# Kernel optimization log

Hardware: AMD Instinct MI355X
Metric: run time of the kernel (lower is better)

The kernel has to match this reference:

```python
import jax, jax.numpy as jnp
import numpy as np

EPS = 1e-5
NEG_SLOPE = 0.01


def _bn_eval(x, gamma, beta, mean, var):
    # x: [B, C, T], per-channel inference batchnorm
    inv = jax.lax.rsqrt(var + EPS)
    return gamma[:, None] * (x - mean[:, None]) * inv[:, None] + beta[:, None]


def _spp_max(x, L, num_levels):
    """Vectorized ragged spatial pyramid max-pool.
    x: [B, C, T] (valid data for sample b lives in [0, L[b]))
    L: [B] int effective lengths (= orig_len - shift)
    Level lvl has W=2**lvl windows: window j covers [j*floor(L/W), j*floor(L/W)+ceil(L/W)),
    matching F.max_pool1d(kernel=ceil(L/W), stride=floor(L/W)).
    Output layout per torch .view(e): channel-major -> [B, C*W] per level, levels concatenated.
    """
    B, C, T = x.shape
    t = jnp.arange(T)
    outs = []
    for lvl in range(num_levels):
        W = 2 ** lvl
        s = L // W                      # stride  = floor(L / 2^lvl)
        k = (L + W - 1) // W            # kernel  = ceil(L / 2^lvl)
        j = jnp.arange(W)
        start = j[None, :] * s[:, None]                        # [B, W]
        end = jnp.minimum(start + k[:, None], L[:, None])      # [B, W]
        m = (t[None, None, :] >= start[:, :, None]) & (t[None, None, :] < end[:, :, None])  # [B, W, T]
        vals = jnp.where(m[:, :, None, :], x[:, None, :, :], -jnp.inf)  # [B, W, C, T]
        pooled = vals.max(axis=-1)                             # [B, W, C]
        outs.append(pooled.transpose(0, 2, 1).reshape(B, C * W))
    return jnp.concatenate(outs, axis=1)


def setup_inputs() -> dict:
    key = jax.random.key(0)
    ks = jax.random.split(key, 8)
    B, C, T, K, n_levels, n_tasks = 32, 128, 8192, 21, 2, 2
    n_lin = 2 * C * (2 ** n_levels - 1)
    x = jax.random.normal(ks[0], (B, C, T), dtype=jnp.float32)
    orig_len = jax.random.randint(ks[1], (B,), 1024, T + 1)
    conv1_w = jax.random.normal(ks[2], (C, C, K), dtype=jnp.float32) * (1.0 / np.sqrt(C * K))
    bn1_gamma = jnp.ones((C,), jnp.float32)
    bn1_beta = jnp.zeros((C,), jnp.float32)
    bn1_mean = jax.random.normal(ks[3], (C,), dtype=jnp.float32) * 0.1
    bn1_var = jax.random.uniform(ks[4], (C,), dtype=jnp.float32, minval=0.5, maxval=1.5)
    fc_w = jax.random.normal(ks[5], (n_tasks, n_lin), dtype=jnp.float32) * (1.0 / np.sqrt(n_lin))
    fc_b = jnp.zeros((n_tasks,), jnp.float32)
    return {"x": x, "orig_len": orig_len, "conv1_w": conv1_w, "bn1_gamma": bn1_gamma,
            "bn1_beta": bn1_beta, "bn1_mean": bn1_mean, "bn1_var": bn1_var,
            "fc_w": fc_w, "fc_b": fc_b}


def reference(x, orig_len, conv1_w, bn1_gamma, bn1_beta, bn1_mean, bn1_var, fc_w, fc_b):
    K = conv1_w.shape[-1]
    n_levels = 2
    # original forward uses conv1/bn1 for BOTH branches (conv2/bn2 dead code)
    h = jax.lax.conv_general_dilated(x, conv1_w, window_strides=(1,), padding='VALID',
                                     dimension_numbers=('NCH', 'OIH', 'NCH'))  # [B, C, T-K+1]
    h = jax.nn.leaky_relu(_bn_eval(h, bn1_gamma, bn1_beta, bn1_mean, bn1_var), NEG_SLOPE)
    x1 = _spp_max(h, orig_len - (K - 1), n_levels)       # spp1: shift = K-1
    x2 = _spp_max(h, orig_len - 2 * (K - 1), n_levels)   # spp2: shift = 2*(K-1)
    feat = jnp.concatenate([x1, x2], axis=1)             # [B, 6C]
    return feat @ fc_w.T + fc_b
```

## Files before the change

kernel.cpp:

```cpp
#include <hip/hip_runtime.h>


typedef __attribute__((ext_vector_type(4))) float f32x4;
typedef __attribute__((ext_vector_type(4))) int i32x4;
typedef unsigned short u16;
typedef unsigned int u32;
typedef signed char i8;

#define T_SZ 8192
#define C_SZ 128
#define B_SZ 32
#define KW 21
#define FEAT 768
#define SX 25.4f
#define IMIN (-2147483647 - 1)

#define XT_OFF  0
#define WP_OFF  33554432u
#define BNA_OFF 33898496u
#define BNB_OFF 33899008u
#define FK_OFF  33899520u
#define PT_OFF  33997824u

__device__ __forceinline__ u32 fkey(float f) {
  u32 u = __float_as_uint(f);
  return (u & 0x80000000u) ? ~u : (u | 0x80000000u);
}
__device__ __forceinline__ float funkey(u32 k) {
  u32 u = (k & 0x80000000u) ? (k ^ 0x80000000u) : ~k;
  return __uint_as_float(u);
}

__device__ __forceinline__ i8 q8(float v) {
  v = fminf(fmaxf(v, -127.f), 127.f);
  return (i8)__float2int_rn(v);
}

__device__ __forceinline__ void gload_lds16(void* lds, const void* g) {
  __builtin_amdgcn_global_load_lds(
      (const __attribute__((address_space(1))) u32*)g,
      (__attribute__((address_space(3))) u32*)lds, 16, 0, 0);
}

__global__ void k_absmax(const float* __restrict__ W, float* __restrict__ parts) {
  const int i0 = ((int)blockIdx.x * 256 + (int)threadIdx.x) * 4;
  float m = 0.f;
#pragma unroll
  for (int j = 0; j < 4; ++j) m = fmaxf(m, fabsf(W[i0 + j]));
#pragma unroll
  for (int d = 1; d < 64; d <<= 1) m = fmaxf(m, __shfl_xor(m, d));
  if ((threadIdx.x & 63) == 0)
    parts[blockIdx.x * 4 + (threadIdx.x >> 6)] = m;
}

__device__ __forceinline__ float reduce_parts(const float* __restrict__ parts,
                                              float* lds4) {
  float m = 0.f;
  for (int i = (int)threadIdx.x; i < 1344; i += 256) m = fmaxf(m, parts[i]);
#pragma unroll
  for (int d = 1; d < 64; d <<= 1) m = fmaxf(m, __shfl_xor(m, d));
  if (((int)threadIdx.x & 63) == 0) lds4[(int)threadIdx.x >> 6] = m;
  __syncthreads();
  return fmaxf(fmaxf(lds4[0], lds4[1]), fmaxf(lds4[2], lds4[3]));
}

__global__ void k_fused(const float* __restrict__ X, const float* __restrict__ W,
                        const float* __restrict__ g, const float* __restrict__ be,
                        const float* __restrict__ mn, const float* __restrict__ vr,
                        const float* __restrict__ parts,
                        i8* __restrict__ Xt, i8* __restrict__ Wp,
                        float* __restrict__ bnA, float* __restrict__ bnB,
                        u32* __restrict__ feat) {
  __shared__ float smem[C_SZ * 65];
  const int tid = (int)threadIdx.x;
  const int bid = (int)blockIdx.x;

  if (bid < 4096) {
    const int b = bid >> 7;
    const int t0 = (bid & 127) * 64;
    const float* Xb = X + (size_t)b * C_SZ * T_SZ;
    {
      const int cw = tid >> 4;
      const int ch = tid & 15;
#pragma unroll
      for (int it = 0; it < 8; ++it) {
        const int ci = it * 16 + cw;
        const f32x4 v = *(const f32x4*)&Xb[(size_t)ci * T_SZ + t0 + ch * 4];
        smem[ci * 65 + ch * 4 + 0] = v.x;
        smem[ci * 65 + ch * 4 + 1] = v.y;
        smem[ci * 65 + ch * 4 + 2] = v.z;
        smem[ci * 65 + ch * 4 + 3] = v.w;
      }
    }
    __syncthreads();
    const int t = tid >> 2;
    const int q = tid & 3;
    u32 dw[8];
#pragma unroll
    for (int d = 0; d < 8; ++d) {
      u32 w = 0;
#pragma unroll
      for (int jb = 0; jb < 4; ++jb) {
        const int j = d * 4 + jb;
        const float v = smem[(q * 32 + j) * 65 + t] * SX;
        w |= ((u32)(unsigned char)q8(v)) << (jb * 8);
      }
      dw[d] = w;
    }
    u32* dst = (u32*)(Xt + ((size_t)(b * T_SZ + t0 + t)) * C_SZ + q * 32);
    *(i32x4*)(dst + 0) = (i32x4){(int)dw[0], (int)dw[1], (int)dw[2], (int)dw[3]};
    *(i32x4*)(dst + 4) = (i32x4){(int)dw[4], (int)dw[5], (int)dw[6], (int)dw[7]};
  } else if (bid == 4096) {
    const float wmax = reduce_parts(parts, smem);
    if (tid < C_SZ) {
      const float sw = 127.f / wmax;
      const float invS = 1.f / (SX * sw);
      float inv = rsqrtf(vr[tid] + 1e-5f);
      float a = g[tid] * inv;
      bnA[tid] = a * invS;
      bnB[tid] = be[tid] - a * mn[tid];
    }
    for (int i = tid; i < B_SZ * FEAT; i += 256) feat[i] = 0u;
  } else {
    const float wmax = reduce_parts(parts, smem);
    const float sw = 127.f / wmax;
    const int i = (bid - 4097) * 256 + tid;
    const int e = i & 15;
    const int lane = (i >> 4) & 63;
    const int f = (i >> 10) & 7;
    const int wr = (i >> 13) & 1;
    const int k = i >> 14;
    const int m = f & 3, ks = f >> 2;
    const int co = wr * 64 + m * 16 + (lane & 15);
    const int ci = ks * 64 + (lane >> 4) * 16 + e;
    Wp[i] = q8(W[(co * C_SZ + ci) * KW + k] * sw);
  }
}

__global__ __launch_bounds__(256, 2)
void k_conv(const i8* __restrict__ Xt, const i8* __restrict__ Wp,
            const float* __restrict__ bnA, const float* __restrict__ bnB,
            const int* __restrict__ olen, u32* __restrict__ feat) {
  __shared__ __align__(16) i8 Xs[280 * C_SZ];
  __shared__ int parti[2][4][C_SZ];

  const int tid = (int)threadIdx.x;
  const int wid = tid >> 6, lane = tid & 63;
  const int wr = wid >> 1, wc = wid & 1;
  const int l4 = lane & 15, lh = lane >> 4;
  const int b = (int)blockIdx.y;
  const int t0 = (int)blockIdx.x * 256;

  i32x4 av[2][4];
  {
    const i8* wb = Wp + ((size_t)wr << 13) + (lane << 4);
#pragma unroll
    for (int f = 0; f < 8; ++f)
      av[f >> 2][f & 3] = *(const i32x4*)&wb[f << 10];
  }

  {
    const i8* xb = Xt + (size_t)b * T_SZ * C_SZ;
    for (int i = wid; i < 35; i += 4) {
      int trow = t0 + i * 8 + (lane >> 3);
      trow = trow < T_SZ ? trow : (T_SZ - 1);
      const i8* src = xb + (size_t)trow * C_SZ + (((lane & 7) ^ (trow & 7)) << 4);
      gload_lds16(&Xs[i * 1024], src);
    }
  }
  __syncthreads();

  i32x4 acc[4][8];
#pragma unroll
  for (int m = 0; m < 4; ++m)
#pragma unroll
    for (int n = 0; n < 8; ++n) acc[m][n] = (i32x4){0, 0, 0, 0};

  const int rowc = wc * 128 + l4;
#pragma unroll 3
  for (int k = 0; k < KW; ++k) {
    const int kn = (k + 1 < KW) ? (k + 1) : k;
    const int rowb = rowc + k;
    const i8* wbn = Wp + (((size_t)(kn * 2 + wr)) << 13) + (lane << 4);
#pragma unroll
    for (int ks = 0; ks < 2; ++ks) {
      const int gran = ((ks << 2) + lh) ^ (rowb & 7);
      const i8* xp = &Xs[(rowb << 7) + (gran << 4)];
      i32x4 bv[8];
#pragma unroll
      for (int n = 0; n < 8; ++n)
        bv[n] = *(const i32x4*)&xp[n << 11];
      __builtin_amdgcn_s_setprio(1);
#pragma unroll
      for (int m = 0; m < 4; ++m)
#pragma unroll
        for (int n = 0; n < 8; ++n)
          acc[m][n] = __builtin_amdgcn_mfma_i32_16x16x64_i8(
              av[ks][m], bv[n], acc[m][n], 0, 0, 0);
      __builtin_amdgcn_s_setprio(0);
#pragma unroll
      for (int m = 0; m < 4; ++m)
        av[ks][m] = *(const i32x4*)&wbn[((ks << 2) + m) << 10];
    }
  }

  const int len = olen[b];
  const int L1 = len - (KW - 1);
  const int L2 = len - 2 * (KW - 1);
  int wlo[4], whi[4];
  wlo[0] = 0;       whi[0] = (L1 + 1) >> 1;
  wlo[1] = L1 >> 1; whi[1] = L1;
  wlo[2] = 0;       whi[2] = (L2 + 1) >> 1;
  wlo[3] = L2 >> 1; whi[3] = L2;

  int tg[8];
#pragma unroll
  for (int n = 0; n < 8; ++n) tg[n] = t0 + wc * 128 + n * 16 + l4;

#pragma unroll
  for (int w = 0; w < 4; ++w) {
    bool pr[8];
#pragma unroll
    for (int n = 0; n < 8; ++n) pr[n] = (tg[n] >= wlo[w]) & (tg[n] < whi[w]);
#pragma unroll
    for (int m = 0; m < 4; ++m)
#pragma unroll
      for (int r = 0; r < 4; ++r) {
        int mx = IMIN;
#pragma unroll
        for (int n = 0; n < 8; ++n)
          mx = max(mx, pr[n] ? acc[m][n][r] : IMIN);
#pragma unroll
        for (int d = 1; d < 16; d <<= 1) mx = max(mx, __shfl_xor(mx, d));
        if (l4 == 0) parti[wc][w][wr * 64 + m * 16 + lh * 4 + r] = mx;
      }
  }
  __syncthreads();
  if (tid < C_SZ) {
    const int c = tid;
    const int v1 = max(parti[0][0][c], parti[1][0][c]);
    const int v2 = max(parti[0][1][c], parti[1][1][c]);
    const int v4 = max(parti[0][2][c], parti[1][2][c]);
    const int v5 = max(parti[0][3][c], parti[1][3][c]);
    const int v0 = max(v1, v2);
    const int v3 = max(v4, v5);
    const float a = bnA[c], bb = bnB[c];
    u32* fb_ = feat + b * FEAT;
    float h;
    h = a * (float)v0 + bb; h = h > 0.f ? h : 0.01f * h;
    atomicMax(&fb_[c], fkey(h));
    h = a * (float)v1 + bb; h = h > 0.f ? h : 0.01f * h;
    atomicMax(&fb_[128 + 2 * c], fkey(h));
    h = a * (float)v2 + bb; h = h > 0.f ? h : 0.01f * h;
    atomicMax(&fb_[129 + 2 * c], fkey(h));
    h = a * (float)v3 + bb; h = h > 0.f ? h : 0.01f * h;
    atomicMax(&fb_[384 + c], fkey(h));
    h = a * (float)v4 + bb; h = h > 0.f ? h : 0.01f * h;
    atomicMax(&fb_[512 + 2 * c], fkey(h));
    h = a * (float)v5 + bb; h = h > 0.f ? h : 0.01f * h;
    atomicMax(&fb_[513 + 2 * c], fkey(h));
  }
}

__global__ void k_fc(const u32* __restrict__ feat, const float* __restrict__ fw,
                     const float* __restrict__ fb, float* __restrict__ out) {
  const int bj = (int)blockIdx.x;
  const int b = bj >> 1, j = bj & 1;
  const int lane = (int)threadIdx.x;
  float s = 0.f;
  for (int i = lane; i < FEAT; i += 64)
    s += funkey(feat[b * FEAT + i]) * fw[j * FEAT + i];
#pragma unroll
  for (int d = 1; d < 64; d <<= 1) s += __shfl_xor(s, d);
  if (lane == 0) out[b * 2 + j] = s + fb[j];
}

extern "C" void kernel_launch(void* const* d_in, const int* in_sizes, int n_in,
                              void* d_out, int out_size, void* d_ws, size_t ws_size,
                              hipStream_t stream) {
  (void)in_sizes; (void)n_in; (void)out_size; (void)ws_size;
  const float* x     = (const float*)d_in[0];
  const int*   olen  = (const int*)d_in[1];
  const float* w     = (const float*)d_in[2];
  const float* gamma = (const float*)d_in[3];
  const float* beta  = (const float*)d_in[4];
  const float* mean  = (const float*)d_in[5];
  const float* var   = (const float*)d_in[6];
  const float* fw    = (const float*)d_in[7];
  const float* fb    = (const float*)d_in[8];
  float* out = (float*)d_out;

  char* ws = (char*)d_ws;
  i8*  Xt    = (i8*)(ws + XT_OFF);
  i8*  Wp    = (i8*)(ws + WP_OFF);
  float* bnA  = (float*)(ws + BNA_OFF);
  float* bnB  = (float*)(ws + BNB_OFF);
  u32* feat  = (u32*)(ws + FK_OFF);
  float* parts = (float*)(ws + PT_OFF);

  k_absmax<<<336, 256, 0, stream>>>(w, parts);
  k_fused<<<4097 + 1344, 256, 0, stream>>>(x, w, gamma, beta, mean, var, parts,
                                           Xt, Wp, bnA, bnB, feat);
  k_conv<<<dim3(T_SZ / 256, B_SZ), 256, 0, stream>>>(Xt, Wp, bnA, bnB, olen, feat);
  k_fc<<<64, 64, 0, stream>>>(feat, fw, fb, out);
}
```

Baseline: 120.1 us.

## Repartition conv waves to cover all output channels over 64 time steps

Changes the wave tiling of the int8 MFMA conv from a 2x2 grid (64 channels x 128 time steps per wave) to four waves each computing all 128 output channels over 64 time steps. Each wave now holds the full weight slice in registers, so the number of LDS reads of the input tile per MFMA is halved. The next-k weight reloads are interleaved into the MFMA loop per row instead of issued after it. In exchange, each wave issues twice as many global weight loads and carries more weight registers, and the partial-max reduction grows from 2 to 4 partials.

```diff
diff --git a/kernel.cpp b/kernel.cpp
--- a/kernel.cpp
+++ b/kernel.cpp
@@ -142,26 +142,27 @@
             const float* __restrict__ bnA, const float* __restrict__ bnB,
             const int* __restrict__ olen, u32* __restrict__ feat) {
   __shared__ __align__(16) i8 Xs[280 * C_SZ];
-  __shared__ int parti[2][4][C_SZ];
+  __shared__ int parti[4][4][C_SZ];
 
   const int tid = (int)threadIdx.x;
-  const int wid = tid >> 6, lane = tid & 63;
-  const int wr = wid >> 1, wc = wid & 1;
+  const int wc = tid >> 6, lane = tid & 63;
   const int l4 = lane & 15, lh = lane >> 4;
   const int b = (int)blockIdx.y;
   const int t0 = (int)blockIdx.x * 256;
 
-  i32x4 av[2][4];
+  i32x4 av[2][8];
   {
-    const i8* wb = Wp + ((size_t)wr << 13) + (lane << 4);
-#pragma unroll
-    for (int f = 0; f < 8; ++f)
-      av[f >> 2][f & 3] = *(const i32x4*)&wb[f << 10];
+    const i8* wb = Wp + (lane << 4);
+#pragma unroll
+    for (int ks = 0; ks < 2; ++ks)
+#pragma unroll
+      for (int m = 0; m < 8; ++m)
+        av[ks][m] = *(const i32x4*)&wb[((m >> 2) << 13) + (((ks << 2) + (m & 3)) << 10)];
   }
 
   {
     const i8* xb = Xt + (size_t)b * T_SZ * C_SZ;
-    for (int i = wid; i < 35; i += 4) {
+    for (int i = wc; i < 35; i += 4) {
       int trow = t0 + i * 8 + (lane >> 3);
       trow = trow < T_SZ ? trow : (T_SZ - 1);
       const i8* src = xb + (size_t)trow * C_SZ + (((lane & 7) ^ (trow & 7)) << 4);
@@ -170,37 +171,37 @@
   }
   __syncthreads();
 
-  i32x4 acc[4][8];
-#pragma unroll
-  for (int m = 0; m < 4; ++m)
-#pragma unroll
-    for (int n = 0; n < 8; ++n) acc[m][n] = (i32x4){0, 0, 0, 0};
-
-  const int rowc = wc * 128 + l4;
+  i32x4 acc[8][4];
+#pragma unroll
+  for (int m = 0; m < 8; ++m)
+#pragma unroll
+    for (int n = 0; n < 4; ++n) acc[m][n] = (i32x4){0, 0, 0, 0};
+
+  const int rowc = wc * 64 + l4;
 #pragma unroll 3
   for (int k = 0; k < KW; ++k) {
     const int kn = (k + 1 < KW) ? (k + 1) : k;
     const int rowb = rowc + k;
-    const i8* wbn = Wp + (((size_t)(kn * 2 + wr)) << 13) + (lane << 4);
+    const i8* wbn = Wp + ((size_t)kn << 14) + (lane << 4);
 #pragma unroll
     for (int ks = 0; ks < 2; ++ks) {
       const int gran = ((ks << 2) + lh) ^ (rowb & 7);
       const i8* xp = &Xs[(rowb << 7) + (gran << 4)];
-      i32x4 bv[8];
-#pragma unroll
-      for (int n = 0; n < 8; ++n)
+      i32x4 bv[4];
+#pragma unroll
+      for (int n = 0; n < 4; ++n)
         bv[n] = *(const i32x4*)&xp[n << 11];
       __builtin_amdgcn_s_setprio(1);
 #pragma unroll
-      for (int m = 0; m < 4; ++m)
-#pragma unroll
-        for (int n = 0; n < 8; ++n)
+      for (int m = 0; m < 8; ++m) {
+#pragma unroll
+        for (int n = 0; n < 4; ++n)
           acc[m][n] = __builtin_amdgcn_mfma_i32_16x16x64_i8(
               av[ks][m], bv[n], acc[m][n], 0, 0, 0);
+        av[ks][m] = *(const i32x4*)&wbn[((m >> 2) << 13) +
+                                        (((ks << 2) + (m & 3)) << 10)];
+      }
       __builtin_amdgcn_s_setprio(0);
-#pragma unroll
-      for (int m = 0; m < 4; ++m)
-        av[ks][m] = *(const i32x4*)&wbn[((ks << 2) + m) << 10];
     }
   }
 
@@ -213,35 +214,39 @@
   wlo[2] = 0;       whi[2] = (L2 + 1) >> 1;
   wlo[3] = L2 >> 1; whi[3] = L2;
 
-  int tg[8];
-#pragma unroll
-  for (int n = 0; n < 8; ++n) tg[n] = t0 + wc * 128 + n * 16 + l4;
+  int tg[4];
+#pragma unroll
+  for (int n = 0; n < 4; ++n) tg[n] = t0 + wc * 64 + n * 16 + l4;
 
 #pragma unroll
   for (int w = 0; w < 4; ++w) {
-    bool pr[8];
-#pragma unroll
-    for (int n = 0; n < 8; ++n) pr[n] = (tg[n] >= wlo[w]) & (tg[n] < whi[w]);
-#pragma unroll
-    for (int m = 0; m < 4; ++m)
+    bool pr[4];
+#pragma unroll
+    for (int n = 0; n < 4; ++n) pr[n] = (tg[n] >= wlo[w]) & (tg[n] < whi[w]);
+#pragma unroll
+    for (int m = 0; m < 8; ++m)
 #pragma unroll
       for (int r = 0; r < 4; ++r) {
         int mx = IMIN;
 #pragma unroll
-        for (int n = 0; n < 8; ++n)
+        for (int n = 0; n < 4; ++n)
           mx = max(mx, pr[n] ? acc[m][n][r] : IMIN);
 #pragma unroll
         for (int d = 1; d < 16; d <<= 1) mx = max(mx, __shfl_xor(mx, d));
-        if (l4 == 0) parti[wc][w][wr * 64 + m * 16 + lh * 4 + r] = mx;
+        if (l4 == 0) parti[wc][w][m * 16 + lh * 4 + r] = mx;
       }
   }
   __syncthreads();
   if (tid < C_SZ) {
     const int c = tid;
-    const int v1 = max(parti[0][0][c], parti[1][0][c]);
-    const int v2 = max(parti[0][1][c], parti[1][1][c]);
-    const int v4 = max(parti[0][2][c], parti[1][2][c]);
-    const int v5 = max(parti[0][3][c], parti[1][3][c]);
+    const int v1 = max(max(parti[0][0][c], parti[1][0][c]),
+                       max(parti[2][0][c], parti[3][0][c]));
+    const int v2 = max(max(parti[0][1][c], parti[1][1][c]),
+                       max(parti[2][1][c], parti[3][1][c]));
+    const int v4 = max(max(parti[0][2][c], parti[1][2][c]),
+                       max(parti[2][2][c], parti[3][2][c]));
+    const int v5 = max(max(parti[0][3][c], parti[1][3][c]),
+                       max(parti[2][3][c], parti[3][3][c]));
     const int v0 = max(v1, v2);
     const int v3 = max(v4, v5);
     const float a = bnA[c], bb = bnB[c];
```

Measured after the change: 138.8 us. 1.16x slower.
